# Kernel optimization log

Measured on AMD Instinct MI355X. Metric: run time of the kernel, lower is better.

## Reference

```python
import jax, jax.numpy as jnp
import numpy as np

INPUT_DIM = 256
RNN_DIM = 256
T, B = 1024, 64


def setup_inputs() -> dict:
    key = jax.random.key(0)
    ks = jax.random.split(key, 12)
    stdv = 1.0 / np.sqrt(RNN_DIM)
    u = lambda k, shape: jax.random.uniform(k, shape, jnp.float32, -stdv, stdv)
    return {
        "input_vectors": jax.random.normal(ks[0], (T, B, INPUT_DIM), jnp.float32),
        "W": u(ks[1], (INPUT_DIM, RNN_DIM)),
        "U": u(ks[2], (RNN_DIM, RNN_DIM)),
        "b": u(ks[3], (1, RNN_DIM)),
        "W_r": u(ks[4], (INPUT_DIM, RNN_DIM)),
        "U_r": u(ks[5], (RNN_DIM, RNN_DIM)),
        "b_r": u(ks[6], (1, RNN_DIM)),
        "W_z": u(ks[7], (INPUT_DIM, RNN_DIM)),
        "U_z": u(ks[8], (RNN_DIM, RNN_DIM)),
        "b_z": u(ks[9], (1, RNN_DIM)),
        "init_hidden": u(ks[10], (1, RNN_DIM)),
    }


def reference(input_vectors, W, U, b, W_r, U_r, b_r, W_z, U_z, b_z, init_hidden):
    # direction='l'. NOTE: the original module appends prev_hidden BEFORE the
    # update, so output[t] is the hidden state entering step t (output[0] is
    # the learned init). Also note the (nonstandard) combine uses (1-r), not
    # (1-z) \u2014 replicated faithfully.
    batch = input_vectors.shape[1]
    h0 = jnp.broadcast_to(init_hidden, (batch, RNN_DIM))

    def step(h, x):  # x: [B, input_dim], h: [B, rnn_dim]
        z = jax.nn.sigmoid(x @ W_z + h @ U_z + b_z)
        r = jax.nn.sigmoid(x @ W_r + h @ U_r + b_r)
        h_bar = jnp.tanh(x @ W + (r * h) @ U + b)
        new_h = (1.0 - r) * h + z * h_bar
        return new_h, h  # emit pre-update hidden, matching the torch code

    _, seq_hidden = jax.lax.scan(step, h0, input_vectors)
    return seq_hidden  # [T, B, rnn_dim]
```

## Files before the change

### kernel.cpp

```cpp
#include <hip/hip_runtime.h>
#include <hip/hip_bf16.h>

typedef __bf16 bf16x8 __attribute__((ext_vector_type(8)));
typedef __bf16 bf16x4 __attribute__((ext_vector_type(4)));
typedef float  f32x4  __attribute__((ext_vector_type(4)));

#define T_STEPS 1024
#define LOG2E 1.4426950408889634f

#define LDS_BARRIER() asm volatile("s_waitcnt lgkmcnt(0)\n\ts_barrier" ::: "memory")

__device__ __forceinline__ float fast_sigmoid(float x) {
  float e = __builtin_amdgcn_exp2f(x * -LOG2E);
  return __builtin_amdgcn_rcpf(1.f + e);
}
__device__ __forceinline__ float fast_tanh(float x) {
  float e = __builtin_amdgcn_exp2f(x * (2.f * LOG2E));
  return 1.f - 2.f * __builtin_amdgcn_rcpf(1.f + e);
}


__global__ __launch_bounds__(256) void prep_frags(
    const float* __restrict__ Wz, const float* __restrict__ Wr, const float* __restrict__ Wh,
    const float* __restrict__ Uz, const float* __restrict__ Ur, const float* __restrict__ Uh,
    __bf16* __restrict__ afrag)
{
  int idx  = blockIdx.x * 256 + threadIdx.x;
  int mat  = idx >> 16;
  int cb   = (idx >> 12) & 15;
  int kblk = (idx >> 9) & 7;
  int l    = (idx >> 3) & 63;
  int j    = idx & 7;
  int k    = kblk * 32 + (l >> 4) * 8 + j;
  int col  = cb * 16 + (l & 15);
  const float* s = (mat == 0) ? Wz : (mat == 1) ? Wr : (mat == 2) ? Wh
                 : (mat == 3) ? Uz : (mat == 4) ? Ur : Uh;
  afrag[idx] = (__bf16)s[k * 256 + col];
}

__global__ __launch_bounds__(256) void gemm_x(
    const float* __restrict__ x, const __bf16* __restrict__ afrag,
    const float* __restrict__ bz, const float* __restrict__ br, const float* __restrict__ bh,
    __bf16* __restrict__ gates)
{
  int t = blockIdx.x;
  int tid = threadIdx.x;
  int l = tid & 63, w = tid >> 6;
  int q = l >> 4, m15 = l & 15;

  bf16x8 bfr[4][8];
#pragma unroll
  for (int g = 0; g < 4; g++) {
    const float* xrow = x + ((size_t)t * 64 + g * 16 + m15) * 256 + q * 8;
#pragma unroll
    for (int kb = 0; kb < 8; kb++) {
      f32x4 lo = *(const f32x4*)(xrow + kb * 32);
      f32x4 hi = *(const f32x4*)(xrow + kb * 32 + 4);
      bf16x8 v;
#pragma unroll
      for (int j = 0; j < 4; j++) { v[j] = (__bf16)lo[j]; v[4 + j] = (__bf16)hi[j]; }
      bfr[g][kb] = v;
    }
  }

  const bf16x8* af = (const bf16x8*)afrag;
#pragma unroll 1
  for (int jj = 0; jj < 12; jj++) {
    int nt = w + 4 * jj;
    int mat = nt >> 4, cb = nt & 15;
    f32x4 acc[4];
#pragma unroll
    for (int g = 0; g < 4; g++) acc[g] = (f32x4){0.f, 0.f, 0.f, 0.f};
#pragma unroll
    for (int kb = 0; kb < 8; kb++) {
      bf16x8 a = af[(nt * 8 + kb) * 64 + l];
#pragma unroll
      for (int g = 0; g < 4; g++)
        acc[g] = __builtin_amdgcn_mfma_f32_16x16x32_bf16(a, bfr[g][kb], acc[g], 0, 0, 0);
    }
    const float* bias = (mat == 0) ? bz : (mat == 1) ? br : bh;
    float b4[4];
#pragma unroll
    for (int i = 0; i < 4; i++) b4[i] = bias[cb * 16 + q * 4 + i];
#pragma unroll
    for (int g = 0; g < 4; g++) {
      bf16x4 ov;
#pragma unroll
      for (int i = 0; i < 4; i++) ov[i] = (__bf16)(acc[g][i] + b4[i]);
      *(bf16x4*)(gates + (((size_t)t * 4 + g) * 48 + nt) * 256 + l * 4) = ov;
    }
  }
}

__global__ __launch_bounds__(512, 2) void gru_rec(
    const __bf16* __restrict__ afrag, const __bf16* __restrict__ gates,
    const float* __restrict__ h0, float* __restrict__ out)
{
  __shared__ bf16x8 hfrag[512];
  __shared__ bf16x8 rhfrag[512];
  int g = blockIdx.x;
  int tid = threadIdx.x;
  int l = tid & 63, w = tid >> 6;
  int q = l >> 4, m15 = l & 15;

  bf16x8 wz[2][8], wr[2][8], wu[2][8];
  const bf16x8* af = (const bf16x8*)afrag;
#pragma unroll
  for (int c = 0; c < 2; c++) {
    int cbg = 2 * w + c;
#pragma unroll
    for (int kb = 0; kb < 8; kb++) {
      wz[c][kb] = af[((3 * 16 + cbg) * 8 + kb) * 64 + l];
      wr[c][kb] = af[((4 * 16 + cbg) * 8 + kb) * 64 + l];
      wu[c][kb] = af[((5 * 16 + cbg) * 8 + kb) * 64 + l];
    }
  }

  float hreg[2][4];
#pragma unroll
  for (int c = 0; c < 2; c++)
#pragma unroll
    for (int i = 0; i < 4; i++)
      hreg[c][i] = h0[32 * w + 16 * c + 4 * q + i];

  {
    const float* hp = h0 + w * 32 + q * 8;
    bf16x8 hv;
#pragma unroll
    for (int j = 0; j < 8; j++) hv[j] = (__bf16)hp[j];
    hfrag[w * 64 + l] = hv;
  }
  LDS_BARRIER();

  int wr0 = w * 128 + (m15 + 16 * (0 + (q >> 1))) * 2 + (q & 1);
  int wr1 = w * 128 + (m15 + 16 * (2 + (q >> 1))) * 2 + (q & 1);
  bf16x4* hf4  = (bf16x4*)hfrag;
  bf16x4* rhf4 = (bf16x4*)rhfrag;

  const size_t STRIDE = (size_t)4 * 48 * 256;
  const __bf16* gz_p = gates + ((size_t)g * 48 + (0 * 16 + 2 * w)) * 256 + l * 4;
  const __bf16* gr_p = gates + ((size_t)g * 48 + (1 * 16 + 2 * w)) * 256 + l * 4;
  const __bf16* gh_p = gates + ((size_t)g * 48 + (2 * 16 + 2 * w)) * 256 + l * 4;
  float* out_p = out + ((size_t)g * 16 + m15) * 256 + 32 * w + 4 * q;

  bf16x4 nz0 = *(const bf16x4*)(gz_p);
  bf16x4 nz1 = *(const bf16x4*)(gz_p + 256);
  bf16x4 nr0 = *(const bf16x4*)(gr_p);
  bf16x4 nr1 = *(const bf16x4*)(gr_p + 256);

#pragma unroll 1
  for (int t = 0; t < T_STEPS; t++) {
    bf16x4 gh0 = *(const bf16x4*)(gh_p);
    bf16x4 gh1 = *(const bf16x4*)(gh_p + 256);
    gh_p += STRIDE;

    {
      f32x4 o0 = {hreg[0][0], hreg[0][1], hreg[0][2], hreg[0][3]};
      f32x4 o1 = {hreg[1][0], hreg[1][1], hreg[1][2], hreg[1][3]};
      *(f32x4*)(out_p)      = o0;
      *(f32x4*)(out_p + 16) = o1;
      out_p += 64 * 256;
    }

    f32x4 az0 = {0,0,0,0}, az1 = {0,0,0,0}, ar0 = {0,0,0,0}, ar1 = {0,0,0,0};
#pragma unroll
    for (int kb = 0; kb < 8; kb++) {
      bf16x8 hb = hfrag[kb * 64 + l];
      az0 = __builtin_amdgcn_mfma_f32_16x16x32_bf16(wz[0][kb], hb, az0, 0, 0, 0);
      az1 = __builtin_amdgcn_mfma_f32_16x16x32_bf16(wz[1][kb], hb, az1, 0, 0, 0);
      ar0 = __builtin_amdgcn_mfma_f32_16x16x32_bf16(wr[0][kb], hb, ar0, 0, 0, 0);
      ar1 = __builtin_amdgcn_mfma_f32_16x16x32_bf16(wr[1][kb], hb, ar1, 0, 0, 0);
    }
    bf16x4 zb0, zb1, rb0, rb1, rh0, rh1;
#pragma unroll
    for (int i = 0; i < 4; i++) {
      float z0 = fast_sigmoid(az0[i] + (float)nz0[i]);
      float z1 = fast_sigmoid(az1[i] + (float)nz1[i]);
      float r0 = fast_sigmoid(ar0[i] + (float)nr0[i]);
      float r1 = fast_sigmoid(ar1[i] + (float)nr1[i]);
      zb0[i] = (__bf16)z0; zb1[i] = (__bf16)z1;
      rb0[i] = (__bf16)r0; rb1[i] = (__bf16)r1;
      rh0[i] = (__bf16)(r0 * hreg[0][i]);
      rh1[i] = (__bf16)(r1 * hreg[1][i]);
    }
    rhf4[wr0] = rh0;
    rhf4[wr1] = rh1;

    {
      size_t adv = (t < T_STEPS - 1) ? STRIDE : 0;
      gz_p += adv; gr_p += adv;
      nz0 = *(const bf16x4*)(gz_p);
      nz1 = *(const bf16x4*)(gz_p + 256);
      nr0 = *(const bf16x4*)(gr_p);
      nr1 = *(const bf16x4*)(gr_p + 256);
    }
    LDS_BARRIER();

    f32x4 ah0 = {0,0,0,0}, ah1 = {0,0,0,0};
#pragma unroll
    for (int kb = 0; kb < 8; kb++) {
      bf16x8 rb = rhfrag[kb * 64 + l];
      ah0 = __builtin_amdgcn_mfma_f32_16x16x32_bf16(wu[0][kb], rb, ah0, 0, 0, 0);
      ah1 = __builtin_amdgcn_mfma_f32_16x16x32_bf16(wu[1][kb], rb, ah1, 0, 0, 0);
    }
    bf16x4 nh0, nh1;
#pragma unroll
    for (int i = 0; i < 4; i++) {
      float hb0 = fast_tanh(ah0[i] + (float)gh0[i]);
      float hb1 = fast_tanh(ah1[i] + (float)gh1[i]);
      float z0 = (float)zb0[i], z1 = (float)zb1[i];
      float r0 = (float)rb0[i], r1 = (float)rb1[i];
      hreg[0][i] = (1.f - r0) * hreg[0][i] + z0 * hb0;
      hreg[1][i] = (1.f - r1) * hreg[1][i] + z1 * hb1;
      nh0[i] = (__bf16)hreg[0][i];
      nh1[i] = (__bf16)hreg[1][i];
    }
    hf4[wr0] = nh0;
    hf4[wr1] = nh1;
    LDS_BARRIER();
  }
}

extern "C" void kernel_launch(void* const* d_in, const int* in_sizes, int n_in,
                              void* d_out, int out_size, void* d_ws, size_t ws_size,
                              hipStream_t stream)
{
  const float* x  = (const float*)d_in[0];
  const float* Wh = (const float*)d_in[1];
  const float* Uh = (const float*)d_in[2];
  const float* bh = (const float*)d_in[3];
  const float* Wr = (const float*)d_in[4];
  const float* Ur = (const float*)d_in[5];
  const float* br = (const float*)d_in[6];
  const float* Wz = (const float*)d_in[7];
  const float* Uz = (const float*)d_in[8];
  const float* bz = (const float*)d_in[9];
  const float* h0 = (const float*)d_in[10];

  __bf16* afrag = (__bf16*)d_ws;
  __bf16* gates = (__bf16*)d_ws + 393216;
  if (ws_size < (size_t)(393216 + 50331648) * 2) return;

  prep_frags<<<1536, 256, 0, stream>>>(Wz, Wr, Wh, Uz, Ur, Uh, afrag);
  gemm_x<<<1024, 256, 0, stream>>>(x, afrag, bz, br, bh, gates);
  gru_rec<<<4, 512, 0, stream>>>(afrag, gates, h0, (float*)d_out);
}
```

Baseline: 2.229 ms.

## Interleave gate layout for 16-byte loads and seed MFMA accumulators with gates

Changes the precomputed gate layout so each lane's two column-block pairs sit contiguously, letting the recurrent kernel fetch z, r and h gate values with single 16-byte loads instead of paired 8-byte loads. The gate values are unpacked from bf16 with bit shifts and used as the initial MFMA accumulators, which removes the separate add after the matrix multiply. The hidden update reuses r*h, computed as h - r*h, so the bf16 r value no longer needs storing and reloading. This shortens the serial per-step critical path at the cost of a slightly different rounding order.

```diff
diff --git a/kernel.cpp b/kernel.cpp
--- a/kernel.cpp
+++ b/kernel.cpp
@@ -4,6 +4,7 @@
 typedef __bf16 bf16x8 __attribute__((ext_vector_type(8)));
 typedef __bf16 bf16x4 __attribute__((ext_vector_type(4)));
 typedef float  f32x4  __attribute__((ext_vector_type(4)));
+typedef unsigned int u32x4 __attribute__((ext_vector_type(4)));
 
 #define T_STEPS 1024
 #define LOG2E 1.4426950408889634f
@@ -18,6 +19,8 @@
   float e = __builtin_amdgcn_exp2f(x * (2.f * LOG2E));
   return 1.f - 2.f * __builtin_amdgcn_rcpf(1.f + e);
 }
+__device__ __forceinline__ float bf_lo(unsigned int u) { return __uint_as_float(u << 16); }
+__device__ __forceinline__ float bf_hi(unsigned int u) { return __uint_as_float(u & 0xFFFF0000u); }
 
 
 __global__ __launch_bounds__(256) void prep_frags(
@@ -82,12 +85,13 @@
     float b4[4];
 #pragma unroll
     for (int i = 0; i < 4; i++) b4[i] = bias[cb * 16 + q * 4 + i];
+    int p = cb >> 1, c = cb & 1;
 #pragma unroll
     for (int g = 0; g < 4; g++) {
       bf16x4 ov;
 #pragma unroll
       for (int i = 0; i < 4; i++) ov[i] = (__bf16)(acc[g][i] + b4[i]);
-      *(bf16x4*)(gates + (((size_t)t * 4 + g) * 48 + nt) * 256 + l * 4) = ov;
+      *(bf16x4*)(gates + ((size_t)t * 4 + g) * 12288 + ((mat * 8 + p) * 64 + l) * 8 + c * 4) = ov;
     }
   }
 }
@@ -137,32 +141,33 @@
   bf16x4* hf4  = (bf16x4*)hfrag;
   bf16x4* rhf4 = (bf16x4*)rhfrag;
 
-  const size_t STRIDE = (size_t)4 * 48 * 256;
-  const __bf16* gz_p = gates + ((size_t)g * 48 + (0 * 16 + 2 * w)) * 256 + l * 4;
-  const __bf16* gr_p = gates + ((size_t)g * 48 + (1 * 16 + 2 * w)) * 256 + l * 4;
-  const __bf16* gh_p = gates + ((size_t)g * 48 + (2 * 16 + 2 * w)) * 256 + l * 4;
-  float* out_p = out + ((size_t)g * 16 + m15) * 256 + 32 * w + 4 * q;
-
-  bf16x4 nz0 = *(const bf16x4*)(gz_p);
-  bf16x4 nz1 = *(const bf16x4*)(gz_p + 256);
-  bf16x4 nr0 = *(const bf16x4*)(gr_p);
-  bf16x4 nr1 = *(const bf16x4*)(gr_p + 256);
+  const int GSTRIDE = 4 * 12288;
+  const __bf16* gt_p = gates + (size_t)g * 12288;
+  int go_z = ((0 * 8 + w) * 64 + l) * 8;
+  int go_r = ((1 * 8 + w) * 64 + l) * 8;
+  int go_h = ((2 * 8 + w) * 64 + l) * 8;
+  const float* out_t = out;
+  int oo = (g * 16 + m15) * 256 + 32 * w + 4 * q;
+
+  u32x4 nzu = *(const u32x4*)(gt_p + go_z);
+  u32x4 nru = *(const u32x4*)(gt_p + go_r);
 
 #pragma unroll 1
   for (int t = 0; t < T_STEPS; t++) {
-    bf16x4 gh0 = *(const bf16x4*)(gh_p);
-    bf16x4 gh1 = *(const bf16x4*)(gh_p + 256);
-    gh_p += STRIDE;
+    u32x4 ghu = *(const u32x4*)(gt_p + go_h);
 
     {
       f32x4 o0 = {hreg[0][0], hreg[0][1], hreg[0][2], hreg[0][3]};
       f32x4 o1 = {hreg[1][0], hreg[1][1], hreg[1][2], hreg[1][3]};
-      *(f32x4*)(out_p)      = o0;
-      *(f32x4*)(out_p + 16) = o1;
-      out_p += 64 * 256;
-    }
-
-    f32x4 az0 = {0,0,0,0}, az1 = {0,0,0,0}, ar0 = {0,0,0,0}, ar1 = {0,0,0,0};
+      *(f32x4*)(out_t + oo)      = o0;
+      *(f32x4*)(out_t + oo + 16) = o1;
+      out_t += 64 * 256;
+    }
+
+    f32x4 az0 = {bf_lo(nzu.x), bf_hi(nzu.x), bf_lo(nzu.y), bf_hi(nzu.y)};
+    f32x4 az1 = {bf_lo(nzu.z), bf_hi(nzu.z), bf_lo(nzu.w), bf_hi(nzu.w)};
+    f32x4 ar0 = {bf_lo(nru.x), bf_hi(nru.x), bf_lo(nru.y), bf_hi(nru.y)};
+    f32x4 ar1 = {bf_lo(nru.z), bf_hi(nru.z), bf_lo(nru.w), bf_hi(nru.w)};
 #pragma unroll
     for (int kb = 0; kb < 8; kb++) {
       bf16x8 hb = hfrag[kb * 64 + l];
@@ -171,32 +176,31 @@
       ar0 = __builtin_amdgcn_mfma_f32_16x16x32_bf16(wr[0][kb], hb, ar0, 0, 0, 0);
       ar1 = __builtin_amdgcn_mfma_f32_16x16x32_bf16(wr[1][kb], hb, ar1, 0, 0, 0);
     }
-    bf16x4 zb0, zb1, rb0, rb1, rh0, rh1;
+    float rhf[2][4];
+    bf16x4 zb0, zb1, rhb0, rhb1;
 #pragma unroll
     for (int i = 0; i < 4; i++) {
-      float z0 = fast_sigmoid(az0[i] + (float)nz0[i]);
-      float z1 = fast_sigmoid(az1[i] + (float)nz1[i]);
-      float r0 = fast_sigmoid(ar0[i] + (float)nr0[i]);
-      float r1 = fast_sigmoid(ar1[i] + (float)nr1[i]);
+      float z0 = fast_sigmoid(az0[i]);
+      float z1 = fast_sigmoid(az1[i]);
+      float r0 = fast_sigmoid(ar0[i]);
+      float r1 = fast_sigmoid(ar1[i]);
       zb0[i] = (__bf16)z0; zb1[i] = (__bf16)z1;
-      rb0[i] = (__bf16)r0; rb1[i] = (__bf16)r1;
-      rh0[i] = (__bf16)(r0 * hreg[0][i]);
-      rh1[i] = (__bf16)(r1 * hreg[1][i]);
-    }
-    rhf4[wr0] = rh0;
-    rhf4[wr1] = rh1;
-
-    {
-      size_t adv = (t < T_STEPS - 1) ? STRIDE : 0;
-      gz_p += adv; gr_p += adv;
-      nz0 = *(const bf16x4*)(gz_p);
-      nz1 = *(const bf16x4*)(gz_p + 256);
-      nr0 = *(const bf16x4*)(gr_p);
-      nr1 = *(const bf16x4*)(gr_p + 256);
-    }
+      rhf[0][i] = r0 * hreg[0][i];
+      rhf[1][i] = r1 * hreg[1][i];
+      rhb0[i] = (__bf16)rhf[0][i];
+      rhb1[i] = (__bf16)rhf[1][i];
+    }
+    rhf4[wr0] = rhb0;
+    rhf4[wr1] = rhb1;
+
+    const __bf16* gn_p = gt_p + ((t < T_STEPS - 1) ? GSTRIDE : 0);
+    nzu = *(const u32x4*)(gn_p + go_z);
+    nru = *(const u32x4*)(gn_p + go_r);
+    gt_p = gn_p;
     LDS_BARRIER();
 
-    f32x4 ah0 = {0,0,0,0}, ah1 = {0,0,0,0};
+    f32x4 ah0 = {bf_lo(ghu.x), bf_hi(ghu.x), bf_lo(ghu.y), bf_hi(ghu.y)};
+    f32x4 ah1 = {bf_lo(ghu.z), bf_hi(ghu.z), bf_lo(ghu.w), bf_hi(ghu.w)};
 #pragma unroll
     for (int kb = 0; kb < 8; kb++) {
       bf16x8 rb = rhfrag[kb * 64 + l];
@@ -206,12 +210,11 @@
     bf16x4 nh0, nh1;
 #pragma unroll
     for (int i = 0; i < 4; i++) {
-      float hb0 = fast_tanh(ah0[i] + (float)gh0[i]);
-      float hb1 = fast_tanh(ah1[i] + (float)gh1[i]);
+      float hb0 = fast_tanh(ah0[i]);
+      float hb1 = fast_tanh(ah1[i]);
       float z0 = (float)zb0[i], z1 = (float)zb1[i];
-      float r0 = (float)rb0[i], r1 = (float)rb1[i];
-      hreg[0][i] = (1.f - r0) * hreg[0][i] + z0 * hb0;
-      hreg[1][i] = (1.f - r1) * hreg[1][i] + z1 * hb1;
+      hreg[0][i] = (hreg[0][i] - rhf[0][i]) + z0 * hb0;
+      hreg[1][i] = (hreg[1][i] - rhf[1][i]) + z1 * hb1;
       nh0[i] = (__bf16)hreg[0][i];
       nh1[i] = (__bf16)hreg[1][i];
     }
```

After: 1.831 ms. -17.8%, faster.
